# Optimization experiments

Hardware: AMD Instinct MI355X
Metric: run time of the kernel (lower is better)

The kernel has to match this reference:

```python
import jax, jax.numpy as jnp
import numpy as np

B, T, C, H = 2, 2048, 1024, 16
DH = C // H
EPS = 1e-5


def _rotary(t_len, d_head):
    inv_freq = 1.0 / (10000.0 ** (jnp.arange(0, d_head, 2, dtype=jnp.float32) / d_head))
    t = jnp.arange(t_len, dtype=jnp.float32)
    freqs = t[:, None] * inv_freq[None, :]           # [T, dh/2]
    emb = jnp.concatenate([freqs, freqs], axis=-1)    # [T, dh]
    return jnp.cos(emb), jnp.sin(emb)


def _apply_rope(x, cos, sin):
    # x: [B,H,T,dh]; cos/sin: [T,dh]
    d = x.shape[-1]
    x1, x2 = x[..., : d // 2], x[..., d // 2 :]
    x_rot = jnp.concatenate([-x2, x1], axis=-1)
    return x * cos + x_rot * sin


def _decay_mask(t_len, n_head):
    gammas = 1.0 - 2.0 ** (-5.0 - jnp.arange(n_head, dtype=jnp.float32))  # [H]
    n = jnp.arange(t_len)[:, None]
    m = jnp.arange(t_len)[None, :]
    dist = n - m
    decay = gammas[:, None, None] ** jnp.maximum(dist, 0).astype(jnp.float32)
    return jnp.where(dist[None] >= 0, decay, 0.0)  # [H,T,T]


def setup_inputs() -> dict:
    key = jax.random.key(0)
    ks = jax.random.split(key, 7)
    s = 1.0 / np.sqrt(C)
    return {
        "x": jax.random.normal(ks[0], (B, T, C), dtype=jnp.float32),
        "Wq": jax.random.normal(ks[1], (C, C), dtype=jnp.float32) * s,
        "Wk": jax.random.normal(ks[2], (C, C), dtype=jnp.float32) * s,
        "Wv": jax.random.normal(ks[3], (C, C), dtype=jnp.float32) * s,
        "Wo": jax.random.normal(ks[4], (C, C), dtype=jnp.float32) * s,
        "gn_weight": jnp.ones((C,), dtype=jnp.float32),
        "gn_bias": jnp.zeros((C,), dtype=jnp.float32),
    }


def reference(x, Wq, Wk, Wv, Wo, gn_weight, gn_bias):
    b, t, c = x.shape
    # projections (torch Linear: y = x @ W.T), split heads -> [B,H,T,dh]
    def proj(W):
        return jnp.einsum("btc,oc->bto", x, W).reshape(b, t, H, DH).transpose(0, 2, 1, 3)
    q, k, v = proj(Wq), proj(Wk), proj(Wv)

    cos, sin = _rotary(t, DH)
    q = _apply_rope(q, cos, sin)
    k = _apply_rope(k, cos, sin)

    decay = _decay_mask(t, H)                          # [H,T,T]
    qk = jnp.einsum("bhtd,bhsd->bhts", q, k) * (1.0 / np.sqrt(DH))
    qk = qk * decay[None]
    out = jnp.einsum("bhts,bhsd->bhtd", qk, v)         # [B,H,T,dh]

    # GroupNorm with n_head groups over channels, per token
    out = out.transpose(0, 2, 1, 3)                    # [B,T,H,dh]
    mu = jnp.mean(out, axis=-1, keepdims=True)
    var = jnp.mean((out - mu) ** 2, axis=-1, keepdims=True)
    out = (out - mu) * jax.lax.rsqrt(var + EPS)
    out = out * gn_weight.reshape(H, DH) + gn_bias.reshape(H, DH)

    out = out.reshape(b, t, c)
    return jnp.einsum("btc,oc->bto", out, Wo)
```

## Files before the change

### kernel.cpp

```cpp
#include <hip/hip_runtime.h>
#include <stdint.h>

#define B_ 2
#define T_ 2048
#define C_ 1024
#define H_ 16
#define DH_ 64
#define M_ (B_*T_)

typedef short bhalf8 __attribute__((ext_vector_type(8)));
typedef float floatx4 __attribute__((ext_vector_type(4)));

__device__ __forceinline__ short f2bf(float f) {
  unsigned u = __float_as_uint(f);
  u += 0x7fffu + ((u >> 16) & 1u);
  return (short)(u >> 16);
}
__device__ __forceinline__ float bf2f(short s) {
  return __uint_as_float(((unsigned)(unsigned short)s) << 16);
}

__device__ __forceinline__ void gll16(void* lds_dst, const void* g_src) {
  __builtin_amdgcn_global_load_lds(
      reinterpret_cast<const uint32_t __attribute__((address_space(1)))*>(
          reinterpret_cast<uintptr_t>(g_src)),
      reinterpret_cast<uint32_t __attribute__((address_space(3)))*>(
          reinterpret_cast<uintptr_t>(lds_dst)),
      16, 0, 0);
}

__global__ void cvt_all(
    const float* __restrict__ x,  const float* __restrict__ wq,
    const float* __restrict__ wk, const float* __restrict__ wv,
    const float* __restrict__ wo,
    short* __restrict__ xb, short* __restrict__ wqb, short* __restrict__ wkb,
    short* __restrict__ wvb, short* __restrict__ wob)
{
  int i = blockIdx.x * blockDim.x + threadIdx.x;
  const float* s; short* d; int off;
  if (i < (M_*C_/4)) { s = x; d = xb; off = i; }
  else {
    int j = i - M_*C_/4;
    int w = j >> 18;
    off = j & ((1<<18) - 1);
    s = (w==0) ? wq : (w==1) ? wk : (w==2) ? wv : wo;
    d = (w==0) ? wqb : (w==1) ? wkb : (w==2) ? wvb : wob;
  }
  float4 v = ((const float4*)s)[off];
  short4 o;
  o.x = f2bf(v.x); o.y = f2bf(v.y); o.z = f2bf(v.z); o.w = f2bf(v.w);
  ((short4*)d)[off] = o;
}

__global__ __launch_bounds__(512, 2) void gemm_qkv(
    const short* __restrict__ X,
    const short* __restrict__ Wq, const short* __restrict__ Wk, const short* __restrict__ Wv,
    short* __restrict__ Qb, short* __restrict__ Kb, short* __restrict__ Vt,
    short* __restrict__ Kt)
{
  __shared__ __align__(16) short SM[4*256*64];
  short (*As)[256*64] = (short (*)[256*64])(SM);
  short (*Bs)[256*64] = (short (*)[256*64])(SM + 2*256*64);
  short* Ct = SM;

  const int tid  = threadIdx.x;
  const int lane = tid & 63;
  const int wid  = tid >> 6;
  const int l15  = lane & 15;
  const int quad = lane >> 4;
  const int wr   = wid >> 2;
  const int wc   = wid & 3;
  const int K    = C_;

  const int bid = blockIdx.x;
  const int wg  = (bid & 7) * 24 + (bid >> 3);
  const int nx  = wg % 12;
  const int m0  = (wg / 12) << 8;

  int kind, nloc;
  const short *Ab, *Bb;
  if (nx < 4)      { kind = 0; nloc = nx << 8;       Ab = X  + (size_t)m0*K;   Bb = Wq + (size_t)nloc*K; }
  else if (nx < 8) { kind = 1; nloc = (nx - 4) << 8; Ab = X  + (size_t)m0*K;   Bb = Wk + (size_t)nloc*K; }
  else             { kind = 2; nloc = (nx - 8) << 8; Ab = Wv + (size_t)nloc*K; Bb = X  + (size_t)m0*K;   }

  const int r_loc = tid >> 3;
  const int g_lin = tid & 7;

  auto stageU = [&](short* lds, const short* g, int q, int k0) {
    int row = (q << 6) + r_loc;
    int gs  = g_lin ^ (row & 7);
    gll16(lds + (q << 12) + (wid << 9), g + (size_t)row * K + k0 + (gs << 3));
  };

  floatx4 acc[8][4] = {};

  stageU(&Bs[0][0], Bb, 0, 0); stageU(&Bs[0][0], Bb, 1, 0);
  stageU(&Bs[0][0], Bb, 2, 0); stageU(&Bs[0][0], Bb, 3, 0);
  stageU(&As[0][0], Ab, 0, 0); stageU(&As[0][0], Ab, 2, 0);
  stageU(&As[0][0], Ab, 1, 0); stageU(&As[0][0], Ab, 3, 0);
  asm volatile("s_waitcnt vmcnt(2)" ::: "memory");
  __builtin_amdgcn_s_barrier();
  __builtin_amdgcn_sched_barrier(0);

  for (int t = 0; t < 16; ++t) {
    const int buf = t & 1, nbuf = buf ^ 1;
    const int kn = (t + 1) << 6;
    const bool pf = (t < 15);
    bhalf8 aF[4], bF[4];

#pragma unroll
    for (int i = 0; i < 4; ++i) {
      int row = (wr << 7) + (i << 4) + l15;
      aF[i] = *(const bhalf8*)&As[buf][(row << 6) + ((quad ^ (row & 7)) << 3)];
    }
#pragma unroll
    for (int n = 0; n < 4; ++n) {
      int row = (wc << 6) + (n << 4) + l15;
      bF[n] = *(const bhalf8*)&Bs[buf][(row << 6) + ((quad ^ (row & 7)) << 3)];
    }
    if (pf) { stageU(&Bs[nbuf][0], Bb, 0, kn); stageU(&Bs[nbuf][0], Bb, 1, kn); }
    __builtin_amdgcn_s_barrier();
    asm volatile("s_waitcnt lgkmcnt(0)" ::: "memory");
    __builtin_amdgcn_sched_barrier(0);
    __builtin_amdgcn_s_setprio(1);
#pragma unroll
    for (int i = 0; i < 4; ++i)
#pragma unroll
      for (int n = 0; n < 4; ++n)
        acc[i][n] = __builtin_amdgcn_mfma_f32_16x16x32_bf16(aF[i], bF[n], acc[i][n], 0, 0, 0);
    __builtin_amdgcn_s_setprio(0);
    asm volatile("s_waitcnt vmcnt(2)" ::: "memory");
    __builtin_amdgcn_s_barrier();
    __builtin_amdgcn_sched_barrier(0);

#pragma unroll
    for (int i = 0; i < 4; ++i) {
      int row = (wr << 7) + ((4 + i) << 4) + l15;
      aF[i] = *(const bhalf8*)&As[buf][(row << 6) + ((quad ^ (row & 7)) << 3)];
    }
    if (pf) { stageU(&Bs[nbuf][0], Bb, 2, kn); stageU(&Bs[nbuf][0], Bb, 3, kn); }
    __builtin_amdgcn_s_barrier();
    asm volatile("s_waitcnt lgkmcnt(0)" ::: "memory");
    __builtin_amdgcn_sched_barrier(0);
    __builtin_amdgcn_s_setprio(1);
#pragma unroll
    for (int i = 0; i < 4; ++i)
#pragma unroll
      for (int n = 0; n < 4; ++n)
        acc[4 + i][n] = __builtin_amdgcn_mfma_f32_16x16x32_bf16(aF[i], bF[n], acc[4 + i][n], 0, 0, 0);
    __builtin_amdgcn_s_setprio(0);
    asm volatile("s_waitcnt vmcnt(4)" ::: "memory");
    __builtin_amdgcn_s_barrier();
    __builtin_amdgcn_sched_barrier(0);

#pragma unroll
    for (int i = 0; i < 4; ++i) {
      int row = (wr << 7) + (i << 4) + l15;
      aF[i] = *(const bhalf8*)&As[buf][(row << 6) + (((4 + quad) ^ (row & 7)) << 3)];
    }
#pragma unroll
    for (int n = 0; n < 4; ++n) {
      int row = (wc << 6) + (n << 4) + l15;
      bF[n] = *(const bhalf8*)&Bs[buf][(row << 6) + (((4 + quad) ^ (row & 7)) << 3)];
    }
    if (pf) { stageU(&As[nbuf][0], Ab, 0, kn); stageU(&As[nbuf][0], Ab, 2, kn); }
    __builtin_amdgcn_s_barrier();
    asm volatile("s_waitcnt lgkmcnt(0)" ::: "memory");
    __builtin_amdgcn_sched_barrier(0);
    __builtin_amdgcn_s_setprio(1);
#pragma unroll
    for (int i = 0; i < 4; ++i)
#pragma unroll
      for (int n = 0; n < 4; ++n)
        acc[i][n] = __builtin_amdgcn_mfma_f32_16x16x32_bf16(aF[i], bF[n], acc[i][n], 0, 0, 0);
    __builtin_amdgcn_s_setprio(0);
    asm volatile("s_waitcnt vmcnt(6)" ::: "memory");
    __builtin_amdgcn_s_barrier();
    __builtin_amdgcn_sched_barrier(0);

#pragma unroll
    for (int i = 0; i < 4; ++i) {
      int row = (wr << 7) + ((4 + i) << 4) + l15;
      aF[i] = *(const bhalf8*)&As[buf][(row << 6) + (((4 + quad) ^ (row & 7)) << 3)];
    }
    if (pf) { stageU(&As[nbuf][0], Ab, 1, kn); stageU(&As[nbuf][0], Ab, 3, kn); }
    __builtin_amdgcn_s_barrier();
    asm volatile("s_waitcnt lgkmcnt(0)" ::: "memory");
    __builtin_amdgcn_sched_barrier(0);
    __builtin_amdgcn_s_setprio(1);
#pragma unroll
    for (int i = 0; i < 4; ++i)
#pragma unroll
      for (int n = 0; n < 4; ++n)
        acc[4 + i][n] = __builtin_amdgcn_mfma_f32_16x16x32_bf16(aF[i], bF[n], acc[4 + i][n], 0, 0, 0);
    __builtin_amdgcn_s_setprio(0);
    asm volatile("s_waitcnt vmcnt(2)" ::: "memory");
    __builtin_amdgcn_s_barrier();
    __builtin_amdgcn_sched_barrier(0);
  }

  if (kind < 2) {
    short* Cb = kind ? Kb : Qb;
    const int hh = (nloc + (wc << 6)) >> 6;
    const float frq0 = exp2f((float)l15        * (-0.4152410118609203f));
    const float frq1 = exp2f((float)(l15 + 16) * (-0.4152410118609203f));
    const int swz = (l15 & 7) << 3;
#pragma unroll
    for (int m = 0; m < 8; ++m)
#pragma unroll
      for (int r = 0; r < 4; ++r) {
        int tl = (wr << 7) + (m << 4) + (quad << 2) + r;
        int n  = m0 + tl;
        int bb = n >> 11, tt = n & (T_ - 1);
        size_t base = ((size_t)(bb * H_ + hh) * T_ + tt) * DH_;
        float tf = (float)tt;
        float v0, v1, v2, v3;
        {
          float ang = tf * frq0;
          float sn = __sinf(ang), cs = __cosf(ang);
          float xlo = acc[m][0][r], xhi = acc[m][2][r];
          v0 = xlo * cs - xhi * sn;
          v1 = xhi * cs + xlo * sn;
          Cb[base + l15]      = f2bf(v0);
          Cb[base + l15 + 32] = f2bf(v1);
        }
        {
          float ang = tf * frq1;
          float sn = __sinf(ang), cs = __cosf(ang);
          float xlo = acc[m][1][r], xhi = acc[m][3][r];
          v2 = xlo * cs - xhi * sn;
          v3 = xhi * cs + xlo * sn;
          Cb[base + l15 + 16] = f2bf(v2);
          Cb[base + l15 + 48] = f2bf(v3);
        }
        if (kind == 1) {
          int tswz = tl ^ swz;
          int cb = (wc << 6);
          Ct[(cb + l15)      * 256 + tswz] = f2bf(v0);
          Ct[(cb + l15 + 32) * 256 + tswz] = f2bf(v1);
          Ct[(cb + l15 + 16) * 256 + tswz] = f2bf(v2);
          Ct[(cb + l15 + 48) * 256 + tswz] = f2bf(v3);
        }
      }
    if (kind == 1) {
      __syncthreads();
      const int hb = nloc >> 6;
#pragma unroll
      for (int rr = 0; rr < 16; ++rr) {
        int lin = rr * 512 + tid;
        int cc_ = lin >> 5;
        int g   = lin & 31;
        bhalf8 v = *(const bhalf8*)&Ct[cc_ * 256 + ((g ^ (cc_ & 7)) << 3)];
        int tg = m0 + (g << 3);
        int bb = tg >> 11, tt = tg & (T_ - 1);
        size_t dst = ((size_t)(bb * H_ + hb + (cc_ >> 6)) * DH_ + (cc_ & 63)) * T_ + tt;
        *(bhalf8*)&Kt[dst] = v;
      }
    }
  } else {
#pragma unroll
    for (int m = 0; m < 8; ++m)
#pragma unroll
      for (int r = 0; r < 4; ++r) {
        int o = nloc + (wr << 7) + (m << 4) + (quad << 2) + r;
#pragma unroll
        for (int n = 0; n < 4; ++n) {
          int tk = m0 + (wc << 6) + (n << 4) + l15;
          int bb = tk >> 11, tt = tk & (T_ - 1);
          Vt[(size_t)bb * (C_ * T_) + (size_t)o * T_ + tt] = f2bf(acc[m][n][r]);
        }
      }
  }
}

__global__ __launch_bounds__(256) void gemm_out(
    const short* __restrict__ A, const short* __restrict__ Bm, float* __restrict__ Cf)
{
  __shared__ __align__(16) short As[3][128*64];
  __shared__ __align__(16) short Bs[3][64*64];
  const int tid = threadIdx.x, lane = tid & 63, wv = tid >> 6;
  const int l15 = lane & 15, quad = lane >> 4;
  const int n0 = blockIdx.x << 6;
  const int m0 = blockIdx.y << 7;

  const short* Ab = A  + (size_t)m0 * C_;
  const short* Bb = Bm + (size_t)n0 * C_;

  auto stage = [&](int buf, int k0) {
#pragma unroll
    for (int i = 0; i < 4; ++i) {
      int slot = (i<<8) + tid, r = slot >> 3, g = (slot & 7) ^ (r & 7);
      gll16(&As[buf][((i<<8) + (wv<<6))*8], Ab + (size_t)r*C_ + k0 + (g<<3));
    }
#pragma unroll
    for (int i = 0; i < 2; ++i) {
      int slot = (i<<8) + tid, r = slot >> 3, g = (slot & 7) ^ (r & 7);
      gll16(&Bs[buf][((i<<8) + (wv<<6))*8], Bb + (size_t)r*C_ + k0 + (g<<3));
    }
  };

  floatx4 acc[2][4] = {};
  stage(0, 0);
  stage(1, 64);
  asm volatile("s_waitcnt vmcnt(6)" ::: "memory");
  __builtin_amdgcn_s_barrier();
  __builtin_amdgcn_sched_barrier(0);

  int cur = 0;
  for (int it = 0; it < 16; ++it) {
    bhalf8 af[2][2], bfr[2][4];
#pragma unroll
    for (int ks = 0; ks < 2; ++ks) {
#pragma unroll
      for (int rt = 0; rt < 2; ++rt) {
        int row = (wv<<5) + rt*16 + l15;
        af[ks][rt] = *(const bhalf8*)&As[cur][(row<<6) + ((((ks<<2)+quad) ^ (row&7))<<3)];
      }
#pragma unroll
      for (int ct = 0; ct < 4; ++ct) {
        int row = ct*16 + l15;
        bfr[ks][ct] = *(const bhalf8*)&Bs[cur][(row<<6) + ((((ks<<2)+quad) ^ (row&7))<<3)];
      }
    }
    const bool pf = (it < 14);
    if (pf) {
      int nb = cur + 2; if (nb >= 3) nb -= 3;
      stage(nb, (it + 2) << 6);
    }
    __builtin_amdgcn_s_barrier();
    asm volatile("s_waitcnt lgkmcnt(0)" ::: "memory");
    __builtin_amdgcn_sched_barrier(0);
    __builtin_amdgcn_s_setprio(1);
#pragma unroll
    for (int ks = 0; ks < 2; ++ks)
#pragma unroll
      for (int rt = 0; rt < 2; ++rt)
#pragma unroll
        for (int ct = 0; ct < 4; ++ct)
          acc[rt][ct] = __builtin_amdgcn_mfma_f32_16x16x32_bf16(af[ks][rt], bfr[ks][ct], acc[rt][ct], 0, 0, 0);
    __builtin_amdgcn_s_setprio(0);
    if (pf) { asm volatile("s_waitcnt vmcnt(6)" ::: "memory"); }
    else    { asm volatile("s_waitcnt vmcnt(0)" ::: "memory"); }
    __builtin_amdgcn_s_barrier();
    __builtin_amdgcn_sched_barrier(0);
    if (++cur == 3) cur = 0;
  }

#pragma unroll
  for (int rt = 0; rt < 2; ++rt)
#pragma unroll
    for (int r = 0; r < 4; ++r) {
      int n = m0 + (wv<<5) + rt*16 + quad*4 + r;
#pragma unroll
      for (int ct = 0; ct < 4; ++ct)
        Cf[(size_t)n * C_ + n0 + ct*16 + l15] = acc[rt][ct][r];
    }
}

__global__ __launch_bounds__(256) void seg_state(
    const short* __restrict__ Kt, const short* __restrict__ Vt,
    short* __restrict__ Pseg, short* __restrict__ Pc)
{
  __shared__ __align__(16) short Ks[2][64*64];
  __shared__ __align__(16) short Vs[2][64*64];
  const int tid = threadIdx.x, lane = tid & 63, wv = tid >> 6;
  const int l15 = lane & 15, quad = lane >> 4;
  const int wrow = wv << 4;
  const int bh = blockIdx.x >> 3, p = blockIdx.x & 7;
  const int h = bh & 15;
  const float log2g = log2f(1.f - exp2f(-5.f - (float)h));
  const float g64 = exp2f(log2g * 64.f);

  float wgt[16];
#pragma unroll
  for (int ks = 0; ks < 2; ++ks)
#pragma unroll
    for (int i = 0; i < 8; ++i)
      wgt[ks*8 + i] = exp2f(log2g * (float)(64 - (ks*32 + (quad<<3) + i)));

  const short* Ktg = Kt + (size_t)bh*DH_*T_;
  const short* Vtg = Vt + (size_t)bh*DH_*T_;

  auto stage = [&](int buf, int jc) {
    const int m0 = ((p<<2) + jc) << 6;
#pragma unroll
    for (int i = 0; i < 2; ++i) {
      int slot = (i<<8) + tid;
      int r = slot >> 3, g = (slot & 7) ^ (r & 7);
      gll16(&Ks[buf][((i<<8) + (wv<<6))*8], Ktg + (size_t)r*T_ + m0 + (g<<3));
      gll16(&Vs[buf][((i<<8) + (wv<<6))*8], Vtg + (size_t)r*T_ + m0 + (g<<3));
    }
  };

  floatx4 acc[4] = {};
  stage(0, 0);
  int cur = 0;
  for (int j = 0; j < 4; ++j) {
    __syncthreads();
    if (j < 3) stage(cur ^ 1, j + 1);
    floatx4 pc[4] = {};
#pragma unroll
    for (int ks = 0; ks < 2; ++ks) {
      int row = wrow + l15;
      bhalf8 va = *(const bhalf8*)&Vs[cur][(row<<6) + ((((ks<<2)+quad) ^ (row&7))<<3)];
      bhalf8 aw;
#pragma unroll
      for (int i = 0; i < 8; ++i) aw[i] = f2bf(bf2f(va[i]) * wgt[ks*8 + i]);
      bhalf8 bk[4];
#pragma unroll
      for (int ct = 0; ct < 4; ++ct) {
        int kr = ct*16 + l15;
        bk[ct] = *(const bhalf8*)&Ks[cur][(kr<<6) + ((((ks<<2)+quad) ^ (kr&7))<<3)];
      }
#pragma unroll
      for (int ct = 0; ct < 4; ++ct)
        pc[ct] = __builtin_amdgcn_mfma_f32_16x16x32_bf16(aw, bk[ct], pc[ct], 0, 0, 0);
    }
#pragma unroll
    for (int ct = 0; ct < 4; ++ct)
#pragma unroll
      for (int r = 0; r < 4; ++r) acc[ct][r] = acc[ct][r]*g64 + pc[ct][r];
    if (j < 3) {
      size_t cbase = (size_t)((bh<<5) + (p<<2) + j) * 2 * 4096;
#pragma unroll
      for (int ct = 0; ct < 4; ++ct)
#pragma unroll
        for (int r = 0; r < 4; ++r) {
          int e = wrow + (quad<<2) + r, d = ct*16 + l15;
          float x = pc[ct][r];
          short hi = f2bf(x);
          short lo = f2bf(x - bf2f(hi));
          Pc[cbase + e*64 + d]        = hi;
          Pc[cbase + 4096 + e*64 + d] = lo;
        }
    }
    cur ^= 1;
  }
  size_t base = (size_t)(bh*8 + p) * 2 * 4096;
#pragma unroll
  for (int ct = 0; ct < 4; ++ct)
#pragma unroll
    for (int r = 0; r < 4; ++r) {
      int e = wrow + (quad<<2) + r, d = ct*16 + l15;
      float x = acc[ct][r];
      short hi = f2bf(x);
      short lo = f2bf(x - bf2f(hi));
      Pseg[base + e*64 + d]        = hi;
      Pseg[base + 4096 + e*64 + d] = lo;
    }
}

__global__ __launch_bounds__(256) void retention_chunk(
    const short* __restrict__ Qb, const short* __restrict__ Kb,
    const short* __restrict__ Vt,
    const short* __restrict__ Pc, const short* __restrict__ Pseg,
    const float* __restrict__ gnw, const float* __restrict__ gnb,
    short* __restrict__ Xn)
{
  __shared__ __align__(16) short Vs[64*64];
  __shared__ __align__(16) short KSs[64*64];
  __shared__ __align__(16) short Sh[64*64];
  __shared__ __align__(16) short Sl[64*64];

  const int tid = threadIdx.x, lane = tid & 63, wv = tid >> 6;
  const int l15 = lane & 15, quad = lane >> 4;
  const int wrow = wv << 4;

  const int idx = blockIdx.x;
  const int bh = idx & 31;
  const int cc = idx >> 5;
  const int c  = ((cc & 7) << 2) | (cc >> 3);
  const int p = c >> 2, j = c & 3;
  const int b = bh >> 4, h = bh & 15;
  const int n0 = c << 6;

  const float log2g = log2f(1.f - exp2f(-5.f - (float)h));

  const short* Kg  = Kb + (size_t)bh*T_*DH_;
  const short* Vtg = Vt + (size_t)bh*DH_*T_;

#pragma unroll
  for (int i = 0; i < 2; ++i) {
    int slot = (i<<8) + tid;
    int r = slot >> 3, g = (slot & 7) ^ (r & 7);
    gll16(&KSs[((i<<8) + (wv<<6))*8], Kg  + (size_t)(n0 + r)*DH_ + (g<<3));
    gll16(&Vs[((i<<8) + (wv<<6))*8],  Vtg + (size_t)r*T_ + n0 + (g<<3));
  }

  const short* Qg = Qb + ((size_t)bh*T_ + n0 + wrow) * DH_;
  bhalf8 aq[2];
#pragma unroll
  for (int ks = 0; ks < 2; ++ks)
    aq[ks] = *(const bhalf8*)(Qg + (size_t)l15*DH_ + ks*32 + quad*8);

  float rowf[4], colf0[4];
#pragma unroll
  for (int r = 0; r < 4; ++r)
    rowf[r] = exp2f(log2g * (float)(wrow + (quad<<2) + r)) * 0.125f;
#pragma unroll
  for (int ct = 0; ct < 4; ++ct)
    colf0[ct] = exp2f(-log2g * (float)(ct*16 + l15));

  const bool has_state = (c > 0);

  floatx4 st[4] = {};
  for (int jp = 0; jp < j; ++jp) {
    float wexp = log2g * (float)((j - 1 - jp) << 6);
    if (wexp < -34.f) continue;
    float w = exp2f(wexp);
    const short* Pg = Pc + (size_t)((bh<<5) + (p<<2) + jp) * 2 * 4096;
#pragma unroll
    for (int ct = 0; ct < 4; ++ct)
#pragma unroll
      for (int r = 0; r < 4; ++r) {
        int e = wrow + (quad<<2) + r, d = ct*16 + l15;
        st[ct][r] += w * (bf2f(Pg[e*64 + d]) + bf2f(Pg[4096 + e*64 + d]));
      }
  }
  for (int pp = 0; pp < p; ++pp) {
    float wexp = log2g * (float)(n0 - ((pp + 1) << 8));
    if (wexp < -34.f) continue;
    float w = exp2f(wexp);
    const short* Pg = Pseg + (size_t)(bh*8 + pp) * 2 * 4096;
#pragma unroll
    for (int ct = 0; ct < 4; ++ct)
#pragma unroll
      for (int r = 0; r < 4; ++r) {
        int e = wrow + (quad<<2) + r, d = ct*16 + l15;
        st[ct][r] += w * (bf2f(Pg[e*64 + d]) + bf2f(Pg[4096 + e*64 + d]));
      }
  }
  if (has_state) {
#pragma unroll
    for (int ct = 0; ct < 4; ++ct)
#pragma unroll
      for (int r = 0; r < 4; ++r) {
        int e = wrow + (quad<<2) + r, d = ct*16 + l15;
        float x = st[ct][r];
        short hi = f2bf(x);
        short lo = f2bf(x - bf2f(hi));
        int addr = (e<<6) + ((((d>>3) ^ (e&7))<<3)) + (d&7);
        Sh[addr] = hi; Sl[addr] = lo;
      }
  }

  __syncthreads();

  floatx4 sacc[4] = {};
#pragma unroll
  for (int ks = 0; ks < 2; ++ks) {
    bhalf8 bk[4];
#pragma unroll
    for (int ct = 0; ct < 4; ++ct) {
      int row = ct*16 + l15;
      bk[ct] = *(const bhalf8*)&KSs[(row<<6) + ((((ks<<2)+quad) ^ (row&7))<<3)];
    }
#pragma unroll
    for (int ct = 0; ct < 4; ++ct)
      sacc[ct] = __builtin_amdgcn_mfma_f32_16x16x32_bf16(aq[ks], bk[ct], sacc[ct], 0, 0, 0);
  }
  __syncthreads();
#pragma unroll
  for (int ct = 0; ct < 4; ++ct) {
    float cf = colf0[ct];
    int colg = (ct<<1) + (l15>>3);
    int m = ct*16 + l15;
#pragma unroll
    for (int r = 0; r < 4; ++r) {
      int row = wrow + (quad<<2) + r;
      float v = (row >= m) ? sacc[ct][r] * (rowf[r] * cf) : 0.f;
      KSs[(row<<6) + ((colg ^ ((row>>1)&7))<<3) + (l15&7)] = f2bf(v);
    }
  }
  floatx4 oacc[4] = {};
#pragma unroll
  for (int ks = 0; ks < 2; ++ks) {
    int row = wrow + l15;
    bhalf8 as_ = *(const bhalf8*)&KSs[(row<<6) + ((((ks<<2)+quad) ^ ((row>>1)&7))<<3)];
    bhalf8 bv[4];
#pragma unroll
    for (int ct = 0; ct < 4; ++ct) {
      int vrow = ct*16 + l15;
      bv[ct] = *(const bhalf8*)&Vs[(vrow<<6) + ((((ks<<2)+quad) ^ (vrow&7))<<3)];
    }
#pragma unroll
    for (int ct = 0; ct < 4; ++ct)
      oacc[ct] = __builtin_amdgcn_mfma_f32_16x16x32_bf16(as_, bv[ct], oacc[ct], 0, 0, 0);
  }

  if (has_state) {
    floatx4 iacc[4] = {};
#pragma unroll
    for (int ks = 0; ks < 2; ++ks) {
      bhalf8 bhf[4], blf[4];
#pragma unroll
      for (int ct = 0; ct < 4; ++ct) {
        int er = ct*16 + l15;
        int ga = ((((ks<<2)+quad) ^ (er&7))<<3);
        bhf[ct] = *(const bhalf8*)&Sh[(er<<6) + ga];
        blf[ct] = *(const bhalf8*)&Sl[(er<<6) + ga];
      }
#pragma unroll
      for (int ct = 0; ct < 4; ++ct) {
        iacc[ct] = __builtin_amdgcn_mfma_f32_16x16x32_bf16(aq[ks], bhf[ct], iacc[ct], 0, 0, 0);
        iacc[ct] = __builtin_amdgcn_mfma_f32_16x16x32_bf16(aq[ks], blf[ct], iacc[ct], 0, 0, 0);
      }
    }
#pragma unroll
    for (int ct = 0; ct < 4; ++ct)
#pragma unroll
      for (int r = 0; r < 4; ++r)
        oacc[ct][r] += rowf[r] * iacc[ct][r];
  }

#pragma unroll
  for (int r = 0; r < 4; ++r) {
    float s1 = oacc[0][r] + oacc[1][r] + oacc[2][r] + oacc[3][r];
    float s2 = oacc[0][r]*oacc[0][r] + oacc[1][r]*oacc[1][r]
             + oacc[2][r]*oacc[2][r] + oacc[3][r]*oacc[3][r];
#pragma unroll
    for (int off = 1; off < 16; off <<= 1) {
      s1 += __shfl_xor(s1, off);
      s2 += __shfl_xor(s2, off);
    }
    float mean = s1 * (1.f/64.f);
    float var  = s2 * (1.f/64.f) - mean*mean;
    float rstd = rsqrtf(var + 1e-5f);
    int t = n0 + wrow + (quad<<2) + r;
    size_t obase = ((size_t)b*T_ + t)*C_ + h*DH_;
#pragma unroll
    for (int ct = 0; ct < 4; ++ct) {
      int d = ct*16 + l15;
      float y = (oacc[ct][r] - mean)*rstd*gnw[h*DH_ + d] + gnb[h*DH_ + d];
      Xn[obase + d] = f2bf(y);
    }
  }
}

extern "C" void kernel_launch(void* const* d_in, const int* in_sizes, int n_in,
                              void* d_out, int out_size, void* d_ws, size_t ws_size,
                              hipStream_t stream) {
  (void)in_sizes; (void)n_in; (void)out_size; (void)ws_size;
  const float* x   = (const float*)d_in[0];
  const float* Wq  = (const float*)d_in[1];
  const float* Wk  = (const float*)d_in[2];
  const float* Wv  = (const float*)d_in[3];
  const float* Wo  = (const float*)d_in[4];
  const float* gnw = (const float*)d_in[5];
  const float* gnb = (const float*)d_in[6];
  float* out = (float*)d_out;

  char* ws = (char*)d_ws;
  short* Xb   = (short*)(ws);
  short* Wqb  = (short*)(ws + (8u<<20));
  short* Pseg = (short*)(ws + (8u<<20));
  short* Wkb  = (short*)(ws + (10u<<20));
  short* Wvb  = (short*)(ws + (12u<<20));
  short* Wob  = (short*)(ws + (14u<<20));
  short* Qb   = (short*)(ws + (16u<<20));
  short* Kb   = (short*)(ws + (24u<<20));
  short* Vtw  = (short*)(ws + (32u<<20));
  short* Xn   = (short*)(ws + (40u<<20));
  short* Ktb  = (short*)(ws + (48u<<20));
  short* Pcb  = (short*)(ws + (64u<<20));

  cvt_all<<<(M_*C_/4 + 4*(C_*C_/4)) / 256, 256, 0, stream>>>(
      x, Wq, Wk, Wv, Wo, Xb, Wqb, Wkb, Wvb, Wob);

  gemm_qkv<<<dim3(192), 512, 0, stream>>>(Xb, Wqb, Wkb, Wvb, Qb, Kb, Vtw, Ktb);
  seg_state<<<256, 256, 0, stream>>>(Ktb, Vtw, Pseg, Pcb);
  retention_chunk<<<1024, 256, 0, stream>>>(Qb, Kb, Vtw, Pcb, Pseg, gnw, gnb, Xn);
  gemm_out<<<dim3(16, 32), 256, 0, stream>>>(Xn, Wob, out);
}
```

Measured before the change: 166.9 us.

## Retile QKV GEMM to 256x192 tiles over concatenated weights with LDS-staged epilogue

The fused QKV projection now treats Wq/Wk/Wv as one contiguous 3072-row weight (Wqb, Wkb, Wvb are adjacent in the workspace) and tiles it as 256 tokens by 192 output channels. That gives 256 workgroups instead of 192, which should fill the 256 CUs better. V is now computed as X·Wv^T instead of Wv·X^T. Every tile goes through an LDS staging buffer, and a unified epilogue applies RoPE and writes Q/K rows, transposed K, or transposed V, with tiles allowed to straddle the Q/K/V boundaries. The risks are more complex epilogue index math, bf16 rounding before RoPE (previously applied in fp32), and narrower per-wave MMA tiles (3 N-fragments instead of 4).

Measured after the change: 202.2 us. 1.21x slower.

```diff
diff --git a/kernel.cpp b/kernel.cpp
--- a/kernel.cpp
+++ b/kernel.cpp
@@ -53,15 +53,14 @@
 }
 
 __global__ __launch_bounds__(512, 2) void gemm_qkv(
-    const short* __restrict__ X,
-    const short* __restrict__ Wq, const short* __restrict__ Wk, const short* __restrict__ Wv,
+    const short* __restrict__ X, const short* __restrict__ Wcat,
     short* __restrict__ Qb, short* __restrict__ Kb, short* __restrict__ Vt,
     short* __restrict__ Kt)
 {
-  __shared__ __align__(16) short SM[4*256*64];
-  short (*As)[256*64] = (short (*)[256*64])(SM);
-  short (*Bs)[256*64] = (short (*)[256*64])(SM + 2*256*64);
-  short* Ct = SM;
+  __shared__ __align__(16) short SM[57344];
+  short* ASb0 = SM;          short* ASb1 = SM + 16384;
+  short* BSb0 = SM + 32768;  short* BSb1 = SM + 45056;
+  short* Ct   = SM;
 
   const int tid  = threadIdx.x;
   const int lane = tid & 63;
@@ -70,55 +69,60 @@
   const int quad = lane >> 4;
   const int wr   = wid >> 2;
   const int wc   = wid & 3;
-  const int K    = C_;
+  const int wcb  = wc * 48;
 
   const int bid = blockIdx.x;
-  const int wg  = (bid & 7) * 24 + (bid >> 3);
-  const int nx  = wg % 12;
-  const int m0  = (wg / 12) << 8;
-
-  int kind, nloc;
-  const short *Ab, *Bb;
-  if (nx < 4)      { kind = 0; nloc = nx << 8;       Ab = X  + (size_t)m0*K;   Bb = Wq + (size_t)nloc*K; }
-  else if (nx < 8) { kind = 1; nloc = (nx - 4) << 8; Ab = X  + (size_t)m0*K;   Bb = Wk + (size_t)nloc*K; }
-  else             { kind = 2; nloc = (nx - 8) << 8; Ab = Wv + (size_t)nloc*K; Bb = X  + (size_t)m0*K;   }
+  const int wg  = (bid & 7) * 32 + (bid >> 3);
+  const int nx  = wg & 15;
+  const int m0  = (wg >> 4) << 8;
+  const int n0g = nx * 192;
+
+  const short* Ab = X    + (size_t)m0 * C_;
+  const short* Bb = Wcat + (size_t)n0g * C_;
 
   const int r_loc = tid >> 3;
   const int g_lin = tid & 7;
 
-  auto stageU = [&](short* lds, const short* g, int q, int k0) {
+  auto stA = [&](short* base, int q, int k0) {
     int row = (q << 6) + r_loc;
     int gs  = g_lin ^ (row & 7);
-    gll16(lds + (q << 12) + (wid << 9), g + (size_t)row * K + k0 + (gs << 3));
+    gll16(base + (q << 12) + (wid << 9), Ab + (size_t)row * C_ + k0 + (gs << 3));
   };
-
-  floatx4 acc[8][4] = {};
-
-  stageU(&Bs[0][0], Bb, 0, 0); stageU(&Bs[0][0], Bb, 1, 0);
-  stageU(&Bs[0][0], Bb, 2, 0); stageU(&Bs[0][0], Bb, 3, 0);
-  stageU(&As[0][0], Ab, 0, 0); stageU(&As[0][0], Ab, 2, 0);
-  stageU(&As[0][0], Ab, 1, 0); stageU(&As[0][0], Ab, 3, 0);
+  auto stB = [&](short* base, int q, int k0) {
+    int row = (q << 6) + r_loc;
+    int gs  = g_lin ^ (row & 7);
+    gll16(base + (q << 12) + (wid << 9), Bb + (size_t)row * C_ + k0 + (gs << 3));
+  };
+
+  floatx4 acc[8][3] = {};
+
+  stB(BSb0, 0, 0); stB(BSb0, 1, 0); stB(BSb0, 2, 0);
+  stA(ASb0, 0, 0); stA(ASb0, 2, 0);
+  stA(ASb0, 1, 0); stA(ASb0, 3, 0);
   asm volatile("s_waitcnt vmcnt(2)" ::: "memory");
   __builtin_amdgcn_s_barrier();
   __builtin_amdgcn_sched_barrier(0);
 
   for (int t = 0; t < 16; ++t) {
-    const int buf = t & 1, nbuf = buf ^ 1;
+    short* Ac = (t & 1) ? ASb1 : ASb0;
+    short* Bc = (t & 1) ? BSb1 : BSb0;
+    short* An = (t & 1) ? ASb0 : ASb1;
+    short* Bn = (t & 1) ? BSb0 : BSb1;
     const int kn = (t + 1) << 6;
     const bool pf = (t < 15);
-    bhalf8 aF[4], bF[4];
+    bhalf8 aF[4], bF[3];
 
 #pragma unroll
     for (int i = 0; i < 4; ++i) {
       int row = (wr << 7) + (i << 4) + l15;
-      aF[i] = *(const bhalf8*)&As[buf][(row << 6) + ((quad ^ (row & 7)) << 3)];
-    }
-#pragma unroll
-    for (int n = 0; n < 4; ++n) {
-      int row = (wc << 6) + (n << 4) + l15;
-      bF[n] = *(const bhalf8*)&Bs[buf][(row << 6) + ((quad ^ (row & 7)) << 3)];
-    }
-    if (pf) { stageU(&Bs[nbuf][0], Bb, 0, kn); stageU(&Bs[nbuf][0], Bb, 1, kn); }
+      aF[i] = *(const bhalf8*)&Ac[(row << 6) + ((quad ^ (row & 7)) << 3)];
+    }
+#pragma unroll
+    for (int n = 0; n < 3; ++n) {
+      int row = wcb + (n << 4) + l15;
+      bF[n] = *(const bhalf8*)&Bc[(row << 6) + ((quad ^ (row & 7)) << 3)];
+    }
+    if (pf) { stB(Bn, 0, kn); stB(Bn, 1, kn); }
     __builtin_amdgcn_s_barrier();
     asm volatile("s_waitcnt lgkmcnt(0)" ::: "memory");
     __builtin_amdgcn_sched_barrier(0);
@@ -126,19 +130,20 @@
 #pragma unroll
     for (int i = 0; i < 4; ++i)
 #pragma unroll
-      for (int n = 0; n < 4; ++n)
+      for (int n = 0; n < 3; ++n)
         acc[i][n] = __builtin_amdgcn_mfma_f32_16x16x32_bf16(aF[i], bF[n], acc[i][n], 0, 0, 0);
     __builtin_amdgcn_s_setprio(0);
-    asm volatile("s_waitcnt vmcnt(2)" ::: "memory");
+    if (pf) { asm volatile("s_waitcnt vmcnt(2)" ::: "memory"); }
+    else    { asm volatile("s_waitcnt vmcnt(0)" ::: "memory"); }
     __builtin_amdgcn_s_barrier();
     __builtin_amdgcn_sched_barrier(0);
 
 #pragma unroll
     for (int i = 0; i < 4; ++i) {
       int row = (wr << 7) + ((4 + i) << 4) + l15;
-      aF[i] = *(const bhalf8*)&As[buf][(row << 6) + ((quad ^ (row & 7)) << 3)];
-    }
-    if (pf) { stageU(&Bs[nbuf][0], Bb, 2, kn); stageU(&Bs[nbuf][0], Bb, 3, kn); }
+      aF[i] = *(const bhalf8*)&Ac[(row << 6) + ((quad ^ (row & 7)) << 3)];
+    }
+    if (pf) { stB(Bn, 2, kn); stA(An, 0, kn); }
     __builtin_amdgcn_s_barrier();
     asm volatile("s_waitcnt lgkmcnt(0)" ::: "memory");
     __builtin_amdgcn_sched_barrier(0);
@@ -146,7 +151,7 @@
 #pragma unroll
     for (int i = 0; i < 4; ++i)
 #pragma unroll
-      for (int n = 0; n < 4; ++n)
+      for (int n = 0; n < 3; ++n)
         acc[4 + i][n] = __builtin_amdgcn_mfma_f32_16x16x32_bf16(aF[i], bF[n], acc[4 + i][n], 0, 0, 0);
     __builtin_amdgcn_s_setprio(0);
     asm volatile("s_waitcnt vmcnt(4)" ::: "memory");
@@ -156,14 +161,14 @@
 #pragma unroll
     for (int i = 0; i < 4; ++i) {
       int row = (wr << 7) + (i << 4) + l15;
-      aF[i] = *(const bhalf8*)&As[buf][(row << 6) + (((4 + quad) ^ (row & 7)) << 3)];
-    }
-#pragma unroll
-    for (int n = 0; n < 4; ++n) {
-      int row = (wc << 6) + (n << 4) + l15;
-      bF[n] = *(const bhalf8*)&Bs[buf][(row << 6) + (((4 + quad) ^ (row & 7)) << 3)];
-    }
-    if (pf) { stageU(&As[nbuf][0], Ab, 0, kn); stageU(&As[nbuf][0], Ab, 2, kn); }
+      aF[i] = *(const bhalf8*)&Ac[(row << 6) + (((4 + quad) ^ (row & 7)) << 3)];
+    }
+#pragma unroll
+    for (int n = 0; n < 3; ++n) {
+      int row = wcb + (n << 4) + l15;
+      bF[n] = *(const bhalf8*)&Bc[(row << 6) + (((4 + quad) ^ (row & 7)) << 3)];
+    }
+    if (pf) { stA(An, 2, kn); }
     __builtin_amdgcn_s_barrier();
     asm volatile("s_waitcnt lgkmcnt(0)" ::: "memory");
     __builtin_amdgcn_sched_barrier(0);
@@ -171,19 +176,19 @@
 #pragma unroll
     for (int i = 0; i < 4; ++i)
 #pragma unroll
-      for (int n = 0; n < 4; ++n)
+      for (int n = 0; n < 3; ++n)
         acc[i][n] = __builtin_amdgcn_mfma_f32_16x16x32_bf16(aF[i], bF[n], acc[i][n], 0, 0, 0);
     __builtin_amdgcn_s_setprio(0);
-    asm volatile("s_waitcnt vmcnt(6)" ::: "memory");
+    asm volatile("s_waitcnt vmcnt(5)" ::: "memory");
     __builtin_amdgcn_s_barrier();
     __builtin_amdgcn_sched_barrier(0);
 
 #pragma unroll
     for (int i = 0; i < 4; ++i) {
       int row = (wr << 7) + ((4 + i) << 4) + l15;
-      aF[i] = *(const bhalf8*)&As[buf][(row << 6) + (((4 + quad) ^ (row & 7)) << 3)];
-    }
-    if (pf) { stageU(&As[nbuf][0], Ab, 1, kn); stageU(&As[nbuf][0], Ab, 3, kn); }
+      aF[i] = *(const bhalf8*)&Ac[(row << 6) + (((4 + quad) ^ (row & 7)) << 3)];
+    }
+    if (pf) { stA(An, 1, kn); stA(An, 3, kn); }
     __builtin_amdgcn_s_barrier();
     asm volatile("s_waitcnt lgkmcnt(0)" ::: "memory");
     __builtin_amdgcn_sched_barrier(0);
@@ -191,7 +196,7 @@
 #pragma unroll
     for (int i = 0; i < 4; ++i)
 #pragma unroll
-      for (int n = 0; n < 4; ++n)
+      for (int n = 0; n < 3; ++n)
         acc[4 + i][n] = __builtin_amdgcn_mfma_f32_16x16x32_bf16(aF[i], bF[n], acc[4 + i][n], 0, 0, 0);
     __builtin_amdgcn_s_setprio(0);
     asm volatile("s_waitcnt vmcnt(2)" ::: "memory");
@@ -199,77 +204,86 @@
     __builtin_amdgcn_sched_barrier(0);
   }
 
-  if (kind < 2) {
-    short* Cb = kind ? Kb : Qb;
-    const int hh = (nloc + (wc << 6)) >> 6;
-    const float frq0 = exp2f((float)l15        * (-0.4152410118609203f));
-    const float frq1 = exp2f((float)(l15 + 16) * (-0.4152410118609203f));
-    const int swz = (l15 & 7) << 3;
-#pragma unroll
-    for (int m = 0; m < 8; ++m)
+#pragma unroll
+  for (int m = 0; m < 8; ++m)
+#pragma unroll
+    for (int n = 0; n < 3; ++n)
 #pragma unroll
       for (int r = 0; r < 4; ++r) {
-        int tl = (wr << 7) + (m << 4) + (quad << 2) + r;
-        int n  = m0 + tl;
-        int bb = n >> 11, tt = n & (T_ - 1);
-        size_t base = ((size_t)(bb * H_ + hh) * T_ + tt) * DH_;
-        float tf = (float)tt;
-        float v0, v1, v2, v3;
-        {
-          float ang = tf * frq0;
+        int tok = (wr << 7) + (m << 4) + (quad << 2) + r;
+        int ch  = wcb + (n << 4) + l15;
+        Ct[tok * 200 + (ch ^ ((tok & 3) << 3))] = f2bf(acc[m][n][r]);
+      }
+  __syncthreads();
+
+  const int bb = m0 >> 11, tbase = m0 & (T_ - 1);
+  const float LAM = -0.4152410118609203f;
+
+  int qkch = 2048 - n0g; qkch = qkch < 0 ? 0 : (qkch > 192 ? 192 : qkch);
+  const int ncg = qkch >> 3;
+  if (ncg > 0) {
+    float fj[8];
+#pragma unroll
+    for (int j = 0; j < 8; ++j) fj[j] = exp2f(LAM * (float)j);
+    const int iters = ncg >> 1;
+    for (int it2 = 0; it2 < iters; ++it2) {
+      int lin = it2 * 512 + tid;
+      int tok, cg;
+      if (ncg == 24) { tok = (lin * 2731) >> 16; cg = lin - tok * 24; }
+      else           { tok = lin >> 4;           cg = lin & 15; }
+      int o0 = n0g + cg * 8;
+      int dh0 = o0 & 63, hh = (o0 & 1023) >> 6, kind = o0 >> 10;
+      int xk = (tok & 3) << 3;
+      bhalf8 va = *(const bhalf8*)&Ct[tok * 200 + ((cg * 8) ^ xk)];
+      bhalf8 vb = *(const bhalf8*)&Ct[tok * 200 + (((cg * 8) ^ 32) ^ xk)];
+      float fb = exp2f(LAM * (float)(dh0 & 31));
+      float tt = (float)(tbase + tok);
+      float sgn = (dh0 < 32) ? -1.f : 1.f;
+      bhalf8 y;
+#pragma unroll
+      for (int j = 0; j < 8; ++j) {
+        float ang = tt * (fb * fj[j]);
+        float sn = __sinf(ang), cs = __cosf(ang);
+        y[j] = f2bf(bf2f(va[j]) * cs + sgn * bf2f(vb[j]) * sn);
+      }
+      short* Cb = kind ? Kb : Qb;
+      *(bhalf8*)&Cb[(((size_t)(bb * H_ + hh)) * T_ + (tbase + tok)) * DH_ + dh0] = y;
+    }
+  }
+
+  int lo = 1024 - n0g; lo = lo < 0 ? 0 : (lo > 192 ? 192 : lo);
+  const int cnt = 192 - lo;
+  if (cnt > 0) {
+    const int iters = cnt >> 4;
+    for (int it2 = 0; it2 < iters; ++it2) {
+      int lin = it2 * 512 + tid;
+      int ch = lo + (lin >> 5), tg = lin & 31;
+      int o = n0g + ch;
+      bhalf8 y;
+      if (o < 2048) {
+        int dh = o & 63, hh = (o & 1023) >> 6;
+        float fb = exp2f(LAM * (float)(dh & 31));
+        float sgn = (dh < 32) ? -1.f : 1.f;
+        int chp = ch ^ 32;
+#pragma unroll
+        for (int j = 0; j < 8; ++j) {
+          int tok = tg * 8 + j; int xk = (tok & 3) << 3;
+          float v  = bf2f(Ct[tok * 200 + (ch  ^ xk)]);
+          float vp = bf2f(Ct[tok * 200 + (chp ^ xk)]);
+          float ang = (float)(tbase + tok) * fb;
           float sn = __sinf(ang), cs = __cosf(ang);
-          float xlo = acc[m][0][r], xhi = acc[m][2][r];
-          v0 = xlo * cs - xhi * sn;
-          v1 = xhi * cs + xlo * sn;
-          Cb[base + l15]      = f2bf(v0);
-          Cb[base + l15 + 32] = f2bf(v1);
+          y[j] = f2bf(v * cs + sgn * vp * sn);
         }
-        {
-          float ang = tf * frq1;
-          float sn = __sinf(ang), cs = __cosf(ang);
-          float xlo = acc[m][1][r], xhi = acc[m][3][r];
-          v2 = xlo * cs - xhi * sn;
-          v3 = xhi * cs + xlo * sn;
-          Cb[base + l15 + 16] = f2bf(v2);
-          Cb[base + l15 + 48] = f2bf(v3);
+        *(bhalf8*)&Kt[(((size_t)(bb * H_ + hh)) * DH_ + dh) * T_ + tbase + tg * 8] = y;
+      } else {
+#pragma unroll
+        for (int j = 0; j < 8; ++j) {
+          int tok = tg * 8 + j; int xk = (tok & 3) << 3;
+          y[j] = Ct[tok * 200 + (ch ^ xk)];
         }
-        if (kind == 1) {
-          int tswz = tl ^ swz;
-          int cb = (wc << 6);
-          Ct[(cb + l15)      * 256 + tswz] = f2bf(v0);
-          Ct[(cb + l15 + 32) * 256 + tswz] = f2bf(v1);
-          Ct[(cb + l15 + 16) * 256 + tswz] = f2bf(v2);
-          Ct[(cb + l15 + 48) * 256 + tswz] = f2bf(v3);
-        }
-      }
-    if (kind == 1) {
-      __syncthreads();
-      const int hb = nloc >> 6;
-#pragma unroll
-      for (int rr = 0; rr < 16; ++rr) {
-        int lin = rr * 512 + tid;
-        int cc_ = lin >> 5;
-        int g   = lin & 31;
-        bhalf8 v = *(const bhalf8*)&Ct[cc_ * 256 + ((g ^ (cc_ & 7)) << 3)];
-        int tg = m0 + (g << 3);
-        int bb = tg >> 11, tt = tg & (T_ - 1);
-        size_t dst = ((size_t)(bb * H_ + hb + (cc_ >> 6)) * DH_ + (cc_ & 63)) * T_ + tt;
-        *(bhalf8*)&Kt[dst] = v;
-      }
-    }
-  } else {
-#pragma unroll
-    for (int m = 0; m < 8; ++m)
-#pragma unroll
-      for (int r = 0; r < 4; ++r) {
-        int o = nloc + (wr << 7) + (m << 4) + (quad << 2) + r;
-#pragma unroll
-        for (int n = 0; n < 4; ++n) {
-          int tk = m0 + (wc << 6) + (n << 4) + l15;
-          int bb = tk >> 11, tt = tk & (T_ - 1);
-          Vt[(size_t)bb * (C_ * T_) + (size_t)o * T_ + tt] = f2bf(acc[m][n][r]);
-        }
-      }
+        *(bhalf8*)&Vt[(size_t)bb * (C_ * T_) + (size_t)(o - 2048) * T_ + tbase + tg * 8] = y;
+      }
+    }
   }
 }
 
@@ -667,7 +681,7 @@
   cvt_all<<<(M_*C_/4 + 4*(C_*C_/4)) / 256, 256, 0, stream>>>(
       x, Wq, Wk, Wv, Wo, Xb, Wqb, Wkb, Wvb, Wob);
 
-  gemm_qkv<<<dim3(192), 512, 0, stream>>>(Xb, Wqb, Wkb, Wvb, Qb, Kb, Vtw, Ktb);
+  gemm_qkv<<<dim3(256), 512, 0, stream>>>(Xb, Wqb, Qb, Kb, Vtw, Ktb);
   seg_state<<<256, 256, 0, stream>>>(Ktb, Vtw, Pseg, Pcb);
   retention_chunk<<<1024, 256, 0, stream>>>(Qb, Kb, Vtw, Pcb, Pseg, gnw, gnb, Xn);
   gemm_out<<<dim3(16, 32), 256, 0, stream>>>(Xn, Wob, out);
```
